# Performance work log

Measured on AMD Instinct MI355X. Metric: run time of the kernel, lower is better.

## Reference

```python
import jax, jax.numpy as jnp
import numpy as np

S, B, D, H, FF, L, V, O = 512, 32, 512, 8, 2048, 6, 32000, 1000
DH = D // H
EPS = 1e-5


def layer_norm(x, g, b):
    mu = jnp.mean(x, axis=-1, keepdims=True)
    var = jnp.mean((x - mu) ** 2, axis=-1, keepdims=True)
    return (x - mu) * jax.lax.rsqrt(var + EPS) * g + b


def positional_encoding(seq_len, dim):
    pos = np.arange(seq_len, dtype=np.float32)[:, None]
    i = np.arange(dim)
    angle = pos / (10000.0 ** ((i // 2 * 2.0) / dim))
    pe = np.where(i % 2 == 0, np.sin(angle), np.cos(angle)).astype(np.float32)
    return jnp.asarray(pe)  # [seq_len, dim]


def setup_inputs() -> dict:
    key = jax.random.key(0)
    ks = jax.random.split(key, 16)
    sc = 0.02
    inp = {
        'x': jax.random.randint(ks[0], (S, B), 0, V, dtype=jnp.int32),
        'x_len': jnp.full((B,), S, dtype=jnp.int32),
        'emb': jax.random.normal(ks[1], (V, D), jnp.float32) * sc,
        'Wq': jax.random.normal(ks[2], (L, D, D), jnp.float32) * sc,
        'bq': jnp.zeros((L, D), jnp.float32),
        'Wk': jax.random.normal(ks[3], (L, D, D), jnp.float32) * sc,
        'bk': jnp.zeros((L, D), jnp.float32),
        'Wv': jax.random.normal(ks[4], (L, D, D), jnp.float32) * sc,
        'bv': jnp.zeros((L, D), jnp.float32),
        'Wo': jax.random.normal(ks[5], (L, D, D), jnp.float32) * sc,
        'bo': jnp.zeros((L, D), jnp.float32),
        'ln1_g': jnp.ones((L, D), jnp.float32),
        'ln1_b': jnp.zeros((L, D), jnp.float32),
        'W1': jax.random.normal(ks[6], (L, D, FF), jnp.float32) * sc,
        'b1': jnp.zeros((L, FF), jnp.float32),
        'W2': jax.random.normal(ks[7], (L, FF, D), jnp.float32) * sc,
        'b2': jnp.zeros((L, D), jnp.float32),
        'ln2_g': jnp.ones((L, D), jnp.float32),
        'ln2_b': jnp.zeros((L, D), jnp.float32),
        'W_fc': jax.random.normal(ks[8], (S * D, O), jnp.float32) * sc,
        'b_fc': jnp.zeros((O,), jnp.float32),
    }
    return inp


def reference(x, x_len, emb, Wq, bq, Wk, bk, Wv, bv, Wo, bo, ln1_g, ln1_b,
              W1, b1, W2, b2, ln2_g, ln2_b, W_fc, b_fc):
    out = emb[x]                      # [S, B, D]
    out = jnp.transpose(out, (1, 0, 2))  # [B, S, D]
    out = out + positional_encoding(S, D)[None, :, :]
    scale = DH ** -0.5
    for l in range(L):
        # NOTE: faithful to the original buggy head-split: plain row-major
        # reshape [B,S,D] -> [B*H,S,DH] without a [B,H,S,DH] transpose.
        q = jnp.reshape(out @ Wq[l] + bq[l], (B * H, S, DH))
        k = jnp.reshape(out @ Wk[l] + bk[l], (B * H, S, DH))
        v = jnp.reshape(out @ Wv[l] + bv[l], (B * H, S, DH))
        attn = jax.nn.softmax(jnp.einsum('gqd,gkd->gqk', q, k) * scale, axis=-1)
        ctx = jnp.einsum('gqk,gkd->gqd', attn, v).reshape(B, S, D)
        h = layer_norm(ctx @ Wo[l] + bo[l] + out, ln1_g[l], ln1_b[l])
        f = jax.nn.relu(h @ W1[l] + b1[l]) @ W2[l] + b2[l]
        out = layer_norm(f + h, ln2_g[l], ln2_b[l])
    out = out.reshape(B, S * D)
    return out @ W_fc + b_fc          # [B, O]
```

## Files before the change

### kernel.cpp

```cpp
#include <hip/hip_runtime.h>
#include <cstdint>
#include <cstddef>

#define S_  512
#define B_  32
#define D_  512
#define FF_ 2048
#define L_  6
#define O_  1000
#define M_  (B_*S_)
#define G_  256
#define DH_ 64

typedef __attribute__((ext_vector_type(8))) short bf16x8;
typedef __attribute__((ext_vector_type(4))) float f32x4;
typedef __attribute__((ext_vector_type(16))) float f32x16;

__device__ __forceinline__ unsigned short f2bf(float f) {
  unsigned int u = __builtin_bit_cast(unsigned int, f);
  u = (u + 0x7fffu + ((u >> 16) & 1u)) >> 16;
  return (unsigned short)u;
}
__device__ __forceinline__ float bf2f(unsigned short u) {
  return __builtin_bit_cast(float, (unsigned int)u << 16);
}
__device__ __forceinline__ unsigned int pkbf(float a, float b) {
  return (unsigned int)f2bf(a) | ((unsigned int)f2bf(b) << 16);
}
__device__ __forceinline__ void gload_lds16(const void* g, void* l) {
  __builtin_amdgcn_global_load_lds(
      (const __attribute__((address_space(1))) unsigned int*)g,
      (__attribute__((address_space(3))) unsigned int*)l, 16, 0, 0);
}

__global__ void pe_kernel(float* __restrict__ pe) {
  int i = blockIdx.x * 256 + threadIdx.x;
  int s = i >> 9, d = i & 511;
  double de = (double)(d & ~1);
  double ang = (double)s * exp(de * (-9.210340371976184 / 512.0));
  pe[i] = (d & 1) ? (float)cos(ang) : (float)sin(ang);
}

__global__ void wconv_kernel(const float* __restrict__ W, unsigned short* __restrict__ Wt,
                             int K, int N, size_t ozs) {
  __shared__ float tile[32][33];
  const float* Wl = W + (size_t)blockIdx.z * K * N;
  unsigned short* Wtl = Wt + (size_t)blockIdx.z * ozs;
  int k0 = blockIdx.x * 32, n0 = blockIdx.y * 32;
  int c = threadIdx.x & 31, rb = threadIdx.x >> 5;
#pragma unroll
  for (int i = 0; i < 4; ++i) {
    int r = rb + i * 8;
    tile[r][c] = Wl[(size_t)(k0 + r) * N + n0 + c];
  }
  __syncthreads();
#pragma unroll
  for (int i = 0; i < 4; ++i) {
    int r = rb + i * 8;
    Wtl[(size_t)(n0 + r) * K + k0 + c] = f2bf(tile[c][r]);
  }
}

__global__ void embed_kernel(const int* __restrict__ x, const float* __restrict__ emb,
                             const float* __restrict__ pe, unsigned short* __restrict__ xb) {
  int bi = blockIdx.x;
  int s = bi / B_, b = bi % B_;
  int tok = x[s * B_ + b];
  int d = threadIdx.x * 4;
  float4 e = *(const float4*)(emb + (size_t)tok * D_ + d);
  float4 p = *(const float4*)(pe + (size_t)s * D_ + d);
  size_t o = ((size_t)b * S_ + s) * D_ + d;
  ushort4 u;
  u.x = f2bf(e.x + p.x); u.y = f2bf(e.y + p.y);
  u.z = f2bf(e.z + p.z); u.w = f2bf(e.w + p.w);
  *(ushort4*)(xb + o) = u;
}

__global__ __launch_bounds__(512) void gemm_kernel(
    const unsigned short* __restrict__ A, const unsigned short* __restrict__ Bt,
    const float* __restrict__ b0, const float* __restrict__ b1, const float* __restrict__ b2,
    unsigned short* __restrict__ o0, unsigned short* __restrict__ o1, unsigned short* __restrict__ o2,
    int K, int N, int relu, int split, int nbx) {
  __shared__ unsigned short As[3][128 * 32];
  __shared__ unsigned short Bs[3][256 * 32];
  int nwg = nbx * (M_ / 128);
  int cpx = nwg >> 3;
  int id = blockIdx.x;
  int wg = (id % 8) * cpx + id / 8;
  int bx = wg % nbx, by = wg / nbx;
  int m0 = by * 128, n0 = bx * 256;

  int tid = threadIdx.x, lane = tid & 63, wid = tid >> 6;
  int wm = wid >> 2, wn = wid & 3;
  f32x4 acc[4][4];
#pragma unroll
  for (int mi = 0; mi < 4; ++mi)
#pragma unroll
    for (int ni = 0; ni < 4; ++ni) acc[mi][ni] = (f32x4)0.0f;

  int srow = lane >> 2, scol = (lane & 3) * 8;
  const unsigned short* Abase = A + (size_t)m0 * K;
  const unsigned short* Bbase = Bt + (size_t)n0 * K;
  int c16 = lane & 15, hi = lane >> 4;
  int koff = hi * 8;
  int arow = wm * 64 + c16, brow = wn * 64 + c16;
  int nk = K >> 5;

  auto STAGE = [&](int kt, int bb) {
    int k0 = kt * 32;
    gload_lds16(Abase + (size_t)(wid * 16 + srow) * K + k0 + scol, (char*)As[bb] + wid * 1024);
#pragma unroll
    for (int i = 0; i < 2; ++i) {
      int c = wid * 2 + i;
      gload_lds16(Bbase + (size_t)(c * 16 + srow) * K + k0 + scol, (char*)Bs[bb] + c * 1024);
    }
  };

  STAGE(0, 0); STAGE(1, 1); STAGE(2, 2);
  int bb = 0;
  for (int kt = 0; kt < nk; ++kt) {
    int rem = nk - 1 - kt;
    if (rem >= 2)      asm volatile("s_waitcnt vmcnt(6)" ::: "memory");
    else if (rem == 1) asm volatile("s_waitcnt vmcnt(3)" ::: "memory");
    else               asm volatile("s_waitcnt vmcnt(0)" ::: "memory");
    __builtin_amdgcn_s_barrier();
    __builtin_amdgcn_sched_barrier(0);
    bf16x8 af[4], bfr[4];
#pragma unroll
    for (int mi = 0; mi < 4; ++mi) af[mi] = *(const bf16x8*)&As[bb][(arow + mi * 16) * 32 + koff];
#pragma unroll
    for (int ni = 0; ni < 4; ++ni) bfr[ni] = *(const bf16x8*)&Bs[bb][(brow + ni * 16) * 32 + koff];
    __builtin_amdgcn_s_setprio(1);
#pragma unroll
    for (int mi = 0; mi < 4; ++mi)
#pragma unroll
      for (int ni = 0; ni < 4; ++ni)
        acc[mi][ni] = __builtin_amdgcn_mfma_f32_16x16x32_bf16(bfr[ni], af[mi], acc[mi][ni], 0, 0, 0);
    __builtin_amdgcn_s_setprio(0);
    __builtin_amdgcn_sched_barrier(0);
    __builtin_amdgcn_s_barrier();
    if (kt + 3 < nk) STAGE(kt + 3, bb);
    bb = (bb == 2) ? 0 : bb + 1;
  }

  const float* bias = b0;
  unsigned short* outb = o0;
  int nbase = n0, ostride = N;
  if (split) {
    int seg = n0 >> 9;
    if (seg == 1) { bias = b1; outb = o1; }
    else if (seg == 2) { bias = b2; outb = o2; }
    nbase = n0 & 511; ostride = 512;
  }
#pragma unroll
  for (int ni = 0; ni < 4; ++ni) {
    int colb = nbase + wn * 64 + ni * 16 + hi * 4;
    float4 bv = *(const float4*)(bias + colb);
#pragma unroll
    for (int mi = 0; mi < 4; ++mi) {
      int row = m0 + wm * 64 + mi * 16 + c16;
      float v0 = acc[mi][ni][0] + bv.x;
      float v1 = acc[mi][ni][1] + bv.y;
      float v2 = acc[mi][ni][2] + bv.z;
      float v3 = acc[mi][ni][3] + bv.w;
      if (relu) { v0 = fmaxf(v0, 0.f); v1 = fmaxf(v1, 0.f); v2 = fmaxf(v2, 0.f); v3 = fmaxf(v3, 0.f); }
      *(uint2*)(outb + (size_t)row * ostride + colb) = make_uint2(pkbf(v0, v1), pkbf(v2, v3));
    }
  }
}

__global__ __launch_bounds__(128) void addln_kernel(
    const unsigned short* __restrict__ Y, const unsigned short* __restrict__ R,
    const float* __restrict__ g, const float* __restrict__ b,
    unsigned short* __restrict__ Out) {
  __shared__ float red[2], red2[2];
  int row = blockIdx.x, t = threadIdx.x;
  size_t o = (size_t)row * 512 + t * 4;
  ushort4 yv = *(const ushort4*)(Y + o);
  ushort4 rv = *(const ushort4*)(R + o);
  float v0 = bf2f(yv.x) + bf2f(rv.x);
  float v1 = bf2f(yv.y) + bf2f(rv.y);
  float v2 = bf2f(yv.z) + bf2f(rv.z);
  float v3 = bf2f(yv.w) + bf2f(rv.w);
  float s = v0 + v1 + v2 + v3;
#pragma unroll
  for (int m = 1; m < 64; m <<= 1) s += __shfl_xor(s, m);
  if ((t & 63) == 0) red[t >> 6] = s;
  __syncthreads();
  float mean = (red[0] + red[1]) * (1.0f / 512.0f);
  float d0 = v0 - mean, d1 = v1 - mean, d2 = v2 - mean, d3 = v3 - mean;
  float sq = d0 * d0 + d1 * d1 + d2 * d2 + d3 * d3;
#pragma unroll
  for (int m = 1; m < 64; m <<= 1) sq += __shfl_xor(sq, m);
  if ((t & 63) == 0) red2[t >> 6] = sq;
  __syncthreads();
  float var = (red2[0] + red2[1]) * (1.0f / 512.0f);
  float rstd = rsqrtf(var + 1e-5f);
  float4 gg = *(const float4*)(g + t * 4);
  float4 bb = *(const float4*)(b + t * 4);
  float y0 = d0 * rstd * gg.x + bb.x;
  float y1 = d1 * rstd * gg.y + bb.y;
  float y2 = d2 * rstd * gg.z + bb.z;
  float y3 = d3 * rstd * gg.w + bb.w;
  *(uint2*)(Out + o) = make_uint2(pkbf(y0, y1), pkbf(y2, y3));
}

__global__ __launch_bounds__(256) void attn_kernel(
    const unsigned short* __restrict__ Q, const unsigned short* __restrict__ Kb,
    const unsigned short* __restrict__ Vb, unsigned short* __restrict__ Ctx) {
  __shared__ char KlB[8192];
  __shared__ char VtB[8192];
  int g = blockIdx.y;
  int q0 = blockIdx.x * 128;
  const unsigned short* Kg = Kb + (size_t)g * 512 * 64;
  const unsigned short* Vg = Vb + (size_t)g * 512 * 64;
  int tid = threadIdx.x, lane = tid & 63, wid = tid >> 6;
  int l31 = lane & 31, h = lane >> 5;
  bool lo = (lane < 32);
  int qrow = q0 + wid * 32 + l31;
  const float sc2 = 0.125f * 1.44269504f;

  bf16x8 qf[4];
  {
    const unsigned short* qp = Q + ((size_t)g * 512 + qrow) * 64;
#pragma unroll
    for (int c = 0; c < 4; ++c) {
      bf16x8 raw = *(const bf16x8*)(qp + c * 16 + h * 8);
      union { unsigned int u[4]; bf16x8 v; } uu;
#pragma unroll
      for (int j = 0; j < 4; ++j)
        uu.u[j] = pkbf(bf2f((unsigned short)raw[2 * j]) * sc2,
                       bf2f((unsigned short)raw[2 * j + 1]) * sc2);
      qf[c] = uu.v;
    }
  }

  f32x16 c0 = (f32x16)0.0f, c1 = (f32x16)0.0f;
  float mr = -3.0e38f, ls = 0.0f;

  for (int kt = 0; kt < 8; ++kt) {
    __syncthreads();
    {
      int row = tid >> 2;
      size_t base = (size_t)(kt * 64 + row) * 64;
#pragma unroll
      for (int i = 0; i < 2; ++i) {
        int cb = ((tid & 3) + 4 * i) * 16;
        bf16x8 kv = *(const bf16x8*)(Kg + base + cb / 2);
        *(bf16x8*)(KlB + row * 128 + (cb ^ ((row & 7) << 4))) = kv;
        bf16x8 vv = *(const bf16x8*)(Vg + base + cb / 2);
#pragma unroll
        for (int j = 0; j < 8; ++j) {
          int d = cb / 2 + j;
          *(unsigned short*)(VtB + d * 128 + ((2 * row) ^ ((d & 7) << 4))) =
              (unsigned short)vv[j];
        }
      }
    }
    __syncthreads();

    f32x16 s0 = (f32x16)0.0f, s1 = (f32x16)0.0f;
#pragma unroll
    for (int c = 0; c < 4; ++c) {
      int cb = 32 * c + 16 * h;
      int sw = cb ^ ((l31 & 7) << 4);
      bf16x8 k0 = *(const bf16x8*)(KlB + l31 * 128 + sw);
      bf16x8 k1 = *(const bf16x8*)(KlB + (32 + l31) * 128 + sw);
      s0 = __builtin_amdgcn_mfma_f32_32x32x16_bf16(k0, qf[c], s0, 0, 0, 0);
      s1 = __builtin_amdgcn_mfma_f32_32x32x16_bf16(k1, qf[c], s1, 0, 0, 0);
    }

    float pm = s0[0];
#pragma unroll
    for (int i = 1; i < 16; ++i) pm = fmaxf(pm, s0[i]);
#pragma unroll
    for (int i = 0; i < 16; ++i) pm = fmaxf(pm, s1[i]);
    pm = fmaxf(pm, __shfl_xor(pm, 32));
    float mnew = fmaxf(mr, pm);
    float alpha = exp2f(mr - mnew);
    mr = mnew;
    float p[32];
    float rs = 0.0f;
#pragma unroll
    for (int i = 0; i < 16; ++i) { p[i] = exp2f(s0[i] - mnew); rs += p[i]; }
#pragma unroll
    for (int i = 0; i < 16; ++i) { p[16 + i] = exp2f(s1[i] - mnew); rs += p[16 + i]; }
    float rso = __shfl_xor(rs, 32);
    ls = ls * alpha + rs + rso;
#pragma unroll
    for (int i = 0; i < 16; ++i) { c0[i] *= alpha; c1[i] *= alpha; }

    union { unsigned int u[4]; bf16x8 v; } pa[4];
#pragma unroll
    for (int t = 0; t < 2; ++t) {
#pragma unroll
      for (int u = 0; u < 2; ++u) {
#pragma unroll
        for (int pr = 0; pr < 2; ++pr) {
          const int b0i = t * 16 + 8 * u;
          unsigned int a  = pkbf(p[b0i + 2 * pr],     p[b0i + 2 * pr + 1]);
          unsigned int b  = pkbf(p[b0i + 4 + 2 * pr], p[b0i + 4 + 2 * pr + 1]);
          unsigned int sa = __shfl_xor(a, 32);
          unsigned int sb = __shfl_xor(b, 32);
          pa[t * 2 + u].u[pr]     = lo ? a  : sb;
          pa[t * 2 + u].u[2 + pr] = lo ? sa : b;
        }
      }
    }

#pragma unroll
    for (int kc = 0; kc < 4; ++kc) {
      int cb = 32 * kc + 16 * h;
      int sw = cb ^ ((l31 & 7) << 4);
      bf16x8 v0 = *(const bf16x8*)(VtB + l31 * 128 + sw);
      bf16x8 v1 = *(const bf16x8*)(VtB + (32 + l31) * 128 + sw);
      c0 = __builtin_amdgcn_mfma_f32_32x32x16_bf16(v0, pa[kc].v, c0, 0, 0, 0);
      c1 = __builtin_amdgcn_mfma_f32_32x32x16_bf16(v1, pa[kc].v, c1, 0, 0, 0);
    }
  }

  float inv = 1.0f / ls;
  unsigned short* cp = Ctx + ((size_t)g * 512 + qrow) * 64;
#pragma unroll
  for (int dh = 0; dh < 2; ++dh) {
#pragma unroll
    for (int rq = 0; rq < 4; ++rq) {
      float e0 = (dh ? c1[rq * 4 + 0] : c0[rq * 4 + 0]) * inv;
      float e1 = (dh ? c1[rq * 4 + 1] : c0[rq * 4 + 1]) * inv;
      float e2 = (dh ? c1[rq * 4 + 2] : c0[rq * 4 + 2]) * inv;
      float e3 = (dh ? c1[rq * 4 + 3] : c0[rq * 4 + 3]) * inv;
      int d0 = dh * 32 + rq * 8 + h * 4;
      *(uint2*)(cp + d0) = make_uint2(pkbf(e0, e1), pkbf(e2, e3));
    }
  }
}

#define KCH 1024
__global__ __launch_bounds__(256) void fc_part_kernel(const unsigned short* __restrict__ act,
                                                      const float* __restrict__ Wfc,
                                                      float* __restrict__ part) {
  __shared__ float al[32][256];
  int o = blockIdx.x * 256 + threadIdx.x;
  int kc = blockIdx.y;
  size_t k0 = (size_t)kc * KCH;
  float acc[32];
#pragma unroll
  for (int bb = 0; bb < 32; ++bb) acc[bb] = 0.0f;
  for (int sub = 0; sub < KCH / 256; ++sub) {
    __syncthreads();
    for (int i = threadIdx.x; i < 32 * 128; i += 256) {
      int bb = i >> 7, kk = (i & 127) * 2;
      ushort2 u = *(const ushort2*)(act + (size_t)bb * 262144 + k0 + sub * 256 + kk);
      al[bb][kk] = bf2f(u.x);
      al[bb][kk + 1] = bf2f(u.y);
    }
    __syncthreads();
    if (o < O_) {
      const float* wp = Wfc + (k0 + sub * 256) * O_ + o;
      for (int kk = 0; kk < 256; ++kk) {
        float w = wp[(size_t)kk * O_];
#pragma unroll
        for (int bb = 0; bb < 32; ++bb) acc[bb] = fmaf(al[bb][kk], w, acc[bb]);
      }
    }
  }
  if (o < O_) {
#pragma unroll
    for (int bb = 0; bb < 32; ++bb) part[((size_t)kc * 32 + bb) * O_ + o] = acc[bb];
  }
}

__global__ void fc_reduce_kernel(const float* __restrict__ part, const float* __restrict__ bfc,
                                 float* __restrict__ out) {
  int o = blockIdx.x * 256 + threadIdx.x;
  int b = blockIdx.y;
  if (o >= O_) return;
  float s = bfc[o];
  for (int c = 0; c < 256; ++c) s += part[((size_t)c * 32 + b) * O_ + o];
  out[(size_t)b * O_ + o] = s;
}

extern "C" void kernel_launch(void* const* d_in, const int* in_sizes, int n_in,
                              void* d_out, int out_size, void* d_ws, size_t ws_size,
                              hipStream_t stream) {
  const int*   x   = (const int*)d_in[0];
  const float* emb = (const float*)d_in[2];
  const float* Wq  = (const float*)d_in[3];
  const float* bq  = (const float*)d_in[4];
  const float* Wk  = (const float*)d_in[5];
  const float* bk  = (const float*)d_in[6];
  const float* Wv  = (const float*)d_in[7];
  const float* bv  = (const float*)d_in[8];
  const float* Wo  = (const float*)d_in[9];
  const float* bo  = (const float*)d_in[10];
  const float* g1  = (const float*)d_in[11];
  const float* bn1 = (const float*)d_in[12];
  const float* W1  = (const float*)d_in[13];
  const float* bf1 = (const float*)d_in[14];
  const float* W2  = (const float*)d_in[15];
  const float* bf2 = (const float*)d_in[16];
  const float* g2  = (const float*)d_in[17];
  const float* bn2 = (const float*)d_in[18];
  const float* Wfc = (const float*)d_in[19];
  const float* bfc = (const float*)d_in[20];
  float* out = (float*)d_out;

  char* ws = (char*)d_ws;
  size_t off = 0;
  auto take = [&](size_t bytes) { char* p = ws + off; off += (bytes + 255) & ~(size_t)255; return p; };
  float*          pe   = (float*)take((size_t)512 * 512 * 4);
  unsigned short* wqkv = (unsigned short*)take((size_t)L_ * 1536 * 512 * 2);
  unsigned short* wot  = (unsigned short*)take((size_t)L_ * 512 * 512 * 2);
  unsigned short* w1t  = (unsigned short*)take((size_t)L_ * 2048 * 512 * 2);
  unsigned short* w2t  = (unsigned short*)take((size_t)L_ * 512 * 2048 * 2);
  unsigned short* xb   = (unsigned short*)take((size_t)M_ * 512 * 2);
  unsigned short* qb   = (unsigned short*)take((size_t)M_ * 512 * 2);
  unsigned short* kb   = (unsigned short*)take((size_t)M_ * 512 * 2);
  unsigned short* vb   = (unsigned short*)take((size_t)M_ * 512 * 2);
  unsigned short* cxb  = (unsigned short*)take((size_t)M_ * 512 * 2);
  unsigned short* hb   = (unsigned short*)take((size_t)M_ * 512 * 2);
  unsigned short* t1   = (unsigned short*)take((size_t)M_ * 512 * 2);
  unsigned short* f1b  = qb;
  float*          part = (float*)qb;

  pe_kernel<<<1024, 256, 0, stream>>>(pe);
  wconv_kernel<<<dim3(16, 16, L_), 256, 0, stream>>>(Wq, wqkv,          512, 512,  (size_t)1536 * 512);
  wconv_kernel<<<dim3(16, 16, L_), 256, 0, stream>>>(Wk, wqkv + 262144, 512, 512,  (size_t)1536 * 512);
  wconv_kernel<<<dim3(16, 16, L_), 256, 0, stream>>>(Wv, wqkv + 524288, 512, 512,  (size_t)1536 * 512);
  wconv_kernel<<<dim3(16, 16, L_), 256, 0, stream>>>(Wo, wot,           512, 512,  (size_t)512 * 512);
  wconv_kernel<<<dim3(16, 64, L_), 256, 0, stream>>>(W1, w1t,           512, 2048, (size_t)2048 * 512);
  wconv_kernel<<<dim3(64, 16, L_), 256, 0, stream>>>(W2, w2t,           2048, 512, (size_t)512 * 2048);
  embed_kernel<<<M_, 128, 0, stream>>>(x, emb, pe, xb);

  for (int l = 0; l < L_; ++l) {
    gemm_kernel<<<768, 512, 0, stream>>>(
        xb, wqkv + (size_t)l * 1536 * 512,
        bq + l * 512, bk + l * 512, bv + l * 512,
        qb, kb, vb, 512, 1536, 0, 1, 6);
    attn_kernel<<<dim3(4, G_), 256, 0, stream>>>(qb, kb, vb, cxb);
    gemm_kernel<<<256, 512, 0, stream>>>(
        cxb, wot + (size_t)l * 512 * 512,
        bo + l * 512, nullptr, nullptr,
        t1, nullptr, nullptr, 512, 512, 0, 0, 2);
    addln_kernel<<<M_, 128, 0, stream>>>(t1, xb, g1 + l * 512, bn1 + l * 512, hb);
    gemm_kernel<<<1024, 512, 0, stream>>>(
        hb, w1t + (size_t)l * 2048 * 512,
        bf1 + l * 2048, nullptr, nullptr,
        f1b, nullptr, nullptr, 512, 2048, 1, 0, 8);
    gemm_kernel<<<256, 512, 0, stream>>>(
        f1b, w2t + (size_t)l * 512 * 2048,
        bf2 + l * 512, nullptr, nullptr,
        t1, nullptr, nullptr, 2048, 512, 0, 0, 2);
    addln_kernel<<<M_, 128, 0, stream>>>(t1, hb, g2 + l * 512, bn2 + l * 512, xb);
  }

  fc_part_kernel<<<dim3(4, 256), 256, 0, stream>>>(xb, Wfc, part);
  fc_reduce_kernel<<<dim3(4, 32), 256, 0, stream>>>(part, bfc, out);
}
```

Baseline: 2.121 ms.

## Enlarge per-warp tiles in GEMM and attention kernels to raise fragment reuse

The GEMM kernel drops from 8 to 4 waves per block while keeping the 128x256 tile, so each wave now computes 128x64 instead of 64x64. The staging loads are redistributed accordingly, and the launch bounds are set to 256 threads with 2 blocks per CU. The attention kernel now has each wave process two 32-row query blocks against the same K/V fragments, halving the grid in the query dimension. Both changes aim to reuse LDS fragments across more MFMAs and cut LDS traffic per FLOP. The cost is higher register pressure and fewer waves per CU, which may reduce latency hiding or cause spills.

```diff
diff --git a/kernel.cpp b/kernel.cpp
--- a/kernel.cpp
+++ b/kernel.cpp
@@ -76,7 +76,7 @@
   *(ushort4*)(xb + o) = u;
 }
 
-__global__ __launch_bounds__(512) void gemm_kernel(
+__global__ __launch_bounds__(256, 2) void gemm_kernel(
     const unsigned short* __restrict__ A, const unsigned short* __restrict__ Bt,
     const float* __restrict__ b0, const float* __restrict__ b1, const float* __restrict__ b2,
     unsigned short* __restrict__ o0, unsigned short* __restrict__ o1, unsigned short* __restrict__ o2,
@@ -86,15 +86,14 @@
   int nwg = nbx * (M_ / 128);
   int cpx = nwg >> 3;
   int id = blockIdx.x;
-  int wg = (id % 8) * cpx + id / 8;
+  int wg = (id & 7) * cpx + (id >> 3);
   int bx = wg % nbx, by = wg / nbx;
   int m0 = by * 128, n0 = bx * 256;
 
   int tid = threadIdx.x, lane = tid & 63, wid = tid >> 6;
-  int wm = wid >> 2, wn = wid & 3;
-  f32x4 acc[4][4];
-#pragma unroll
-  for (int mi = 0; mi < 4; ++mi)
+  f32x4 acc[8][4];
+#pragma unroll
+  for (int mi = 0; mi < 8; ++mi)
 #pragma unroll
     for (int ni = 0; ni < 4; ++ni) acc[mi][ni] = (f32x4)0.0f;
 
@@ -103,16 +102,20 @@
   const unsigned short* Bbase = Bt + (size_t)n0 * K;
   int c16 = lane & 15, hi = lane >> 4;
   int koff = hi * 8;
-  int arow = wm * 64 + c16, brow = wn * 64 + c16;
+  int brow = wid * 64 + c16;
   int nk = K >> 5;
 
   auto STAGE = [&](int kt, int bb) {
     int k0 = kt * 32;
-    gload_lds16(Abase + (size_t)(wid * 16 + srow) * K + k0 + scol, (char*)As[bb] + wid * 1024);
-#pragma unroll
-    for (int i = 0; i < 2; ++i) {
-      int c = wid * 2 + i;
-      gload_lds16(Bbase + (size_t)(c * 16 + srow) * K + k0 + scol, (char*)Bs[bb] + c * 1024);
+#pragma unroll
+    for (int i = 0; i < 6; ++i) {
+      int c = wid * 6 + i;
+      if (c < 8) {
+        gload_lds16(Abase + (size_t)(c * 16 + srow) * K + k0 + scol, (char*)As[bb] + c * 1024);
+      } else {
+        int c2 = c - 8;
+        gload_lds16(Bbase + (size_t)(c2 * 16 + srow) * K + k0 + scol, (char*)Bs[bb] + c2 * 1024);
+      }
     }
   };
 
@@ -120,19 +123,19 @@
   int bb = 0;
   for (int kt = 0; kt < nk; ++kt) {
     int rem = nk - 1 - kt;
-    if (rem >= 2)      asm volatile("s_waitcnt vmcnt(6)" ::: "memory");
-    else if (rem == 1) asm volatile("s_waitcnt vmcnt(3)" ::: "memory");
+    if (rem >= 2)      asm volatile("s_waitcnt vmcnt(12)" ::: "memory");
+    else if (rem == 1) asm volatile("s_waitcnt vmcnt(6)" ::: "memory");
     else               asm volatile("s_waitcnt vmcnt(0)" ::: "memory");
     __builtin_amdgcn_s_barrier();
     __builtin_amdgcn_sched_barrier(0);
-    bf16x8 af[4], bfr[4];
-#pragma unroll
-    for (int mi = 0; mi < 4; ++mi) af[mi] = *(const bf16x8*)&As[bb][(arow + mi * 16) * 32 + koff];
+    bf16x8 af[8], bfr[4];
+#pragma unroll
+    for (int mi = 0; mi < 8; ++mi) af[mi] = *(const bf16x8*)&As[bb][(mi * 16 + c16) * 32 + koff];
 #pragma unroll
     for (int ni = 0; ni < 4; ++ni) bfr[ni] = *(const bf16x8*)&Bs[bb][(brow + ni * 16) * 32 + koff];
     __builtin_amdgcn_s_setprio(1);
 #pragma unroll
-    for (int mi = 0; mi < 4; ++mi)
+    for (int mi = 0; mi < 8; ++mi)
 #pragma unroll
       for (int ni = 0; ni < 4; ++ni)
         acc[mi][ni] = __builtin_amdgcn_mfma_f32_16x16x32_bf16(bfr[ni], af[mi], acc[mi][ni], 0, 0, 0);
@@ -154,11 +157,11 @@
   }
 #pragma unroll
   for (int ni = 0; ni < 4; ++ni) {
-    int colb = nbase + wn * 64 + ni * 16 + hi * 4;
+    int colb = nbase + wid * 64 + ni * 16 + hi * 4;
     float4 bv = *(const float4*)(bias + colb);
 #pragma unroll
-    for (int mi = 0; mi < 4; ++mi) {
-      int row = m0 + wm * 64 + mi * 16 + c16;
+    for (int mi = 0; mi < 8; ++mi) {
+      int row = m0 + mi * 16 + c16;
       float v0 = acc[mi][ni][0] + bv.x;
       float v1 = acc[mi][ni][1] + bv.y;
       float v2 = acc[mi][ni][2] + bv.z;
@@ -211,32 +214,40 @@
   __shared__ char KlB[8192];
   __shared__ char VtB[8192];
   int g = blockIdx.y;
-  int q0 = blockIdx.x * 128;
+  int q0 = blockIdx.x * 256;
   const unsigned short* Kg = Kb + (size_t)g * 512 * 64;
   const unsigned short* Vg = Vb + (size_t)g * 512 * 64;
   int tid = threadIdx.x, lane = tid & 63, wid = tid >> 6;
   int l31 = lane & 31, h = lane >> 5;
   bool lo = (lane < 32);
-  int qrow = q0 + wid * 32 + l31;
+  int qrowA = q0 + wid * 64 + l31;
+  int qrowB = qrowA + 32;
   const float sc2 = 0.125f * 1.44269504f;
 
-  bf16x8 qf[4];
+  bf16x8 qfa[4], qfb[4];
   {
-    const unsigned short* qp = Q + ((size_t)g * 512 + qrow) * 64;
+    const unsigned short* qpa = Q + ((size_t)g * 512 + qrowA) * 64;
+    const unsigned short* qpb = Q + ((size_t)g * 512 + qrowB) * 64;
 #pragma unroll
     for (int c = 0; c < 4; ++c) {
-      bf16x8 raw = *(const bf16x8*)(qp + c * 16 + h * 8);
-      union { unsigned int u[4]; bf16x8 v; } uu;
-#pragma unroll
-      for (int j = 0; j < 4; ++j)
-        uu.u[j] = pkbf(bf2f((unsigned short)raw[2 * j]) * sc2,
-                       bf2f((unsigned short)raw[2 * j + 1]) * sc2);
-      qf[c] = uu.v;
-    }
-  }
-
-  f32x16 c0 = (f32x16)0.0f, c1 = (f32x16)0.0f;
-  float mr = -3.0e38f, ls = 0.0f;
+      bf16x8 ra = *(const bf16x8*)(qpa + c * 16 + h * 8);
+      bf16x8 rb = *(const bf16x8*)(qpb + c * 16 + h * 8);
+      union { unsigned int u[4]; bf16x8 v; } ua, ub;
+#pragma unroll
+      for (int j = 0; j < 4; ++j) {
+        ua.u[j] = pkbf(bf2f((unsigned short)ra[2 * j]) * sc2,
+                       bf2f((unsigned short)ra[2 * j + 1]) * sc2);
+        ub.u[j] = pkbf(bf2f((unsigned short)rb[2 * j]) * sc2,
+                       bf2f((unsigned short)rb[2 * j + 1]) * sc2);
+      }
+      qfa[c] = ua.v; qfb[c] = ub.v;
+    }
+  }
+
+  f32x16 cA0 = (f32x16)0.0f, cA1 = (f32x16)0.0f;
+  f32x16 cB0 = (f32x16)0.0f, cB1 = (f32x16)0.0f;
+  float mrA = -3.0e38f, lsA = 0.0f;
+  float mrB = -3.0e38f, lsB = 0.0f;
 
   for (int kt = 0; kt < 8; ++kt) {
     __syncthreads();
@@ -259,78 +270,98 @@
     }
     __syncthreads();
 
-    f32x16 s0 = (f32x16)0.0f, s1 = (f32x16)0.0f;
-#pragma unroll
-    for (int c = 0; c < 4; ++c) {
-      int cb = 32 * c + 16 * h;
-      int sw = cb ^ ((l31 & 7) << 4);
-      bf16x8 k0 = *(const bf16x8*)(KlB + l31 * 128 + sw);
-      bf16x8 k1 = *(const bf16x8*)(KlB + (32 + l31) * 128 + sw);
-      s0 = __builtin_amdgcn_mfma_f32_32x32x16_bf16(k0, qf[c], s0, 0, 0, 0);
-      s1 = __builtin_amdgcn_mfma_f32_32x32x16_bf16(k1, qf[c], s1, 0, 0, 0);
-    }
-
-    float pm = s0[0];
-#pragma unroll
-    for (int i = 1; i < 16; ++i) pm = fmaxf(pm, s0[i]);
-#pragma unroll
-    for (int i = 0; i < 16; ++i) pm = fmaxf(pm, s1[i]);
-    pm = fmaxf(pm, __shfl_xor(pm, 32));
-    float mnew = fmaxf(mr, pm);
-    float alpha = exp2f(mr - mnew);
-    mr = mnew;
-    float p[32];
-    float rs = 0.0f;
-#pragma unroll
-    for (int i = 0; i < 16; ++i) { p[i] = exp2f(s0[i] - mnew); rs += p[i]; }
-#pragma unroll
-    for (int i = 0; i < 16; ++i) { p[16 + i] = exp2f(s1[i] - mnew); rs += p[16 + i]; }
-    float rso = __shfl_xor(rs, 32);
-    ls = ls * alpha + rs + rso;
-#pragma unroll
-    for (int i = 0; i < 16; ++i) { c0[i] *= alpha; c1[i] *= alpha; }
-
-    union { unsigned int u[4]; bf16x8 v; } pa[4];
-#pragma unroll
-    for (int t = 0; t < 2; ++t) {
-#pragma unroll
-      for (int u = 0; u < 2; ++u) {
-#pragma unroll
-        for (int pr = 0; pr < 2; ++pr) {
-          const int b0i = t * 16 + 8 * u;
-          unsigned int a  = pkbf(p[b0i + 2 * pr],     p[b0i + 2 * pr + 1]);
-          unsigned int b  = pkbf(p[b0i + 4 + 2 * pr], p[b0i + 4 + 2 * pr + 1]);
-          unsigned int sa = __shfl_xor(a, 32);
-          unsigned int sb = __shfl_xor(b, 32);
-          pa[t * 2 + u].u[pr]     = lo ? a  : sb;
-          pa[t * 2 + u].u[2 + pr] = lo ? sa : b;
+#pragma unroll
+    for (int sub = 0; sub < 2; ++sub) {
+      f32x16 s0 = (f32x16)0.0f, s1 = (f32x16)0.0f;
+#pragma unroll
+      for (int c = 0; c < 4; ++c) {
+        int cb = 32 * c + 16 * h;
+        int sw = cb ^ ((l31 & 7) << 4);
+        bf16x8 k0 = *(const bf16x8*)(KlB + l31 * 128 + sw);
+        bf16x8 k1 = *(const bf16x8*)(KlB + (32 + l31) * 128 + sw);
+        bf16x8 qf = sub ? qfb[c] : qfa[c];
+        s0 = __builtin_amdgcn_mfma_f32_32x32x16_bf16(k0, qf, s0, 0, 0, 0);
+        s1 = __builtin_amdgcn_mfma_f32_32x32x16_bf16(k1, qf, s1, 0, 0, 0);
+      }
+
+      float mr = sub ? mrB : mrA;
+      float ls = sub ? lsB : lsA;
+      float pm = s0[0];
+#pragma unroll
+      for (int i = 1; i < 16; ++i) pm = fmaxf(pm, s0[i]);
+#pragma unroll
+      for (int i = 0; i < 16; ++i) pm = fmaxf(pm, s1[i]);
+      pm = fmaxf(pm, __shfl_xor(pm, 32));
+      float mnew = fmaxf(mr, pm);
+      float alpha = exp2f(mr - mnew);
+      float p[32];
+      float rs = 0.0f;
+#pragma unroll
+      for (int i = 0; i < 16; ++i) { p[i] = exp2f(s0[i] - mnew); rs += p[i]; }
+#pragma unroll
+      for (int i = 0; i < 16; ++i) { p[16 + i] = exp2f(s1[i] - mnew); rs += p[16 + i]; }
+      float rso = __shfl_xor(rs, 32);
+      ls = ls * alpha + rs + rso;
+      if (sub) { mrB = mnew; lsB = ls; } else { mrA = mnew; lsA = ls; }
+      if (sub) {
+#pragma unroll
+        for (int i = 0; i < 16; ++i) { cB0[i] *= alpha; cB1[i] *= alpha; }
+      } else {
+#pragma unroll
+        for (int i = 0; i < 16; ++i) { cA0[i] *= alpha; cA1[i] *= alpha; }
+      }
+
+      union { unsigned int u[4]; bf16x8 v; } pa[4];
+#pragma unroll
+      for (int t = 0; t < 2; ++t) {
+#pragma unroll
+        for (int u = 0; u < 2; ++u) {
+#pragma unroll
+          for (int pr = 0; pr < 2; ++pr) {
+            const int b0i = t * 16 + 8 * u;
+            unsigned int a  = pkbf(p[b0i + 2 * pr],     p[b0i + 2 * pr + 1]);
+            unsigned int b  = pkbf(p[b0i + 4 + 2 * pr], p[b0i + 4 + 2 * pr + 1]);
+            unsigned int sa = __shfl_xor(a, 32);
+            unsigned int sb = __shfl_xor(b, 32);
+            pa[t * 2 + u].u[pr]     = lo ? a  : sb;
+            pa[t * 2 + u].u[2 + pr] = lo ? sa : b;
+          }
         }
       }
-    }
-
-#pragma unroll
-    for (int kc = 0; kc < 4; ++kc) {
-      int cb = 32 * kc + 16 * h;
-      int sw = cb ^ ((l31 & 7) << 4);
-      bf16x8 v0 = *(const bf16x8*)(VtB + l31 * 128 + sw);
-      bf16x8 v1 = *(const bf16x8*)(VtB + (32 + l31) * 128 + sw);
-      c0 = __builtin_amdgcn_mfma_f32_32x32x16_bf16(v0, pa[kc].v, c0, 0, 0, 0);
-      c1 = __builtin_amdgcn_mfma_f32_32x32x16_bf16(v1, pa[kc].v, c1, 0, 0, 0);
-    }
-  }
-
-  float inv = 1.0f / ls;
-  unsigned short* cp = Ctx + ((size_t)g * 512 + qrow) * 64;
-#pragma unroll
-  for (int dh = 0; dh < 2; ++dh) {
-#pragma unroll
-    for (int rq = 0; rq < 4; ++rq) {
-      float e0 = (dh ? c1[rq * 4 + 0] : c0[rq * 4 + 0]) * inv;
-      float e1 = (dh ? c1[rq * 4 + 1] : c0[rq * 4 + 1]) * inv;
-      float e2 = (dh ? c1[rq * 4 + 2] : c0[rq * 4 + 2]) * inv;
-      float e3 = (dh ? c1[rq * 4 + 3] : c0[rq * 4 + 3]) * inv;
-      int d0 = dh * 32 + rq * 8 + h * 4;
-      *(uint2*)(cp + d0) = make_uint2(pkbf(e0, e1), pkbf(e2, e3));
+
+#pragma unroll
+      for (int kc = 0; kc < 4; ++kc) {
+        int cb = 32 * kc + 16 * h;
+        int sw = cb ^ ((l31 & 7) << 4);
+        bf16x8 v0 = *(const bf16x8*)(VtB + l31 * 128 + sw);
+        bf16x8 v1 = *(const bf16x8*)(VtB + (32 + l31) * 128 + sw);
+        if (sub) {
+          cB0 = __builtin_amdgcn_mfma_f32_32x32x16_bf16(v0, pa[kc].v, cB0, 0, 0, 0);
+          cB1 = __builtin_amdgcn_mfma_f32_32x32x16_bf16(v1, pa[kc].v, cB1, 0, 0, 0);
+        } else {
+          cA0 = __builtin_amdgcn_mfma_f32_32x32x16_bf16(v0, pa[kc].v, cA0, 0, 0, 0);
+          cA1 = __builtin_amdgcn_mfma_f32_32x32x16_bf16(v1, pa[kc].v, cA1, 0, 0, 0);
+        }
+      }
+    }
+  }
+
+#pragma unroll
+  for (int sub = 0; sub < 2; ++sub) {
+    float inv = 1.0f / (sub ? lsB : lsA);
+    int qrow = sub ? qrowB : qrowA;
+    unsigned short* cp = Ctx + ((size_t)g * 512 + qrow) * 64;
+#pragma unroll
+    for (int dh = 0; dh < 2; ++dh) {
+#pragma unroll
+      for (int rq = 0; rq < 4; ++rq) {
+        float e0 = (sub ? (dh ? cB1[rq * 4 + 0] : cB0[rq * 4 + 0]) : (dh ? cA1[rq * 4 + 0] : cA0[rq * 4 + 0])) * inv;
+        float e1 = (sub ? (dh ? cB1[rq * 4 + 1] : cB0[rq * 4 + 1]) : (dh ? cA1[rq * 4 + 1] : cA0[rq * 4 + 1])) * inv;
+        float e2 = (sub ? (dh ? cB1[rq * 4 + 2] : cB0[rq * 4 + 2]) : (dh ? cA1[rq * 4 + 2] : cA0[rq * 4 + 2])) * inv;
+        float e3 = (sub ? (dh ? cB1[rq * 4 + 3] : cB0[rq * 4 + 3]) : (dh ? cA1[rq * 4 + 3] : cA0[rq * 4 + 3])) * inv;
+        int d0 = dh * 32 + rq * 8 + h * 4;
+        *(uint2*)(cp + d0) = make_uint2(pkbf(e0, e1), pkbf(e2, e3));
+      }
     }
   }
 }
@@ -433,21 +464,21 @@
   embed_kernel<<<M_, 128, 0, stream>>>(x, emb, pe, xb);
 
   for (int l = 0; l < L_; ++l) {
-    gemm_kernel<<<768, 512, 0, stream>>>(
+    gemm_kernel<<<768, 256, 0, stream>>>(
         xb, wqkv + (size_t)l * 1536 * 512,
         bq + l * 512, bk + l * 512, bv + l * 512,
         qb, kb, vb, 512, 1536, 0, 1, 6);
-    attn_kernel<<<dim3(4, G_), 256, 0, stream>>>(qb, kb, vb, cxb);
-    gemm_kernel<<<256, 512, 0, stream>>>(
+    attn_kernel<<<dim3(2, G_), 256, 0, stream>>>(qb, kb, vb, cxb);
+    gemm_kernel<<<256, 256, 0, stream>>>(
         cxb, wot + (size_t)l * 512 * 512,
         bo + l * 512, nullptr, nullptr,
         t1, nullptr, nullptr, 512, 512, 0, 0, 2);
     addln_kernel<<<M_, 128, 0, stream>>>(t1, xb, g1 + l * 512, bn1 + l * 512, hb);
-    gemm_kernel<<<1024, 512, 0, stream>>>(
+    gemm_kernel<<<1024, 256, 0, stream>>>(
         hb, w1t + (size_t)l * 2048 * 512,
         bf1 + l * 2048, nullptr, nullptr,
         f1b, nullptr, nullptr, 512, 2048, 1, 0, 8);
-    gemm_kernel<<<256, 512, 0, stream>>>(
+    gemm_kernel<<<256, 256, 0, stream>>>(
         f1b, w2t + (size_t)l * 512 * 2048,
         bf2 + l * 512, nullptr, nullptr,
         t1, nullptr, nullptr, 2048, 512, 0, 0, 2);
```

Result: no change. 2.121 ms (+0.0%).
